# Optimization experiments

Hardware: AMD Instinct MI355X
Metric: run time of the kernel (lower is better)

## Reference

```python
import jax, jax.numpy as jnp
import numpy as np
import itertools

B = 2; DIM = 256; HEADS = 8; RES = 256; WIN = 16
FWS = WIN // 2            # freq window size = 8
HD = DIM // HEADS         # head dim = 32
N = FWS * FWS             # tokens per window = 64
SCALE = HD ** -0.5

def _make_bias_idxs():
    pts = list(itertools.product(range(FWS), range(FWS)))
    offs, idxs = {}, []
    for p1 in pts:
        for p2 in pts:
            o = (abs(p1[0] - p2[0]), abs(p1[1] - p2[1]))
            if o not in offs:
                offs[o] = len(offs)
            idxs.append(offs[o])
    return np.asarray(idxs, np.int32).reshape(N, N), len(offs)

def _conv(x, w, stride, pad, groups, lhs_dilation=None):
    return jax.lax.conv_general_dilated(
        x, w, (stride, stride), pad, lhs_dilation=lhs_dilation,
        feature_group_count=groups, dimension_numbers=('NCHW', 'OIHW', 'NCHW'))

def _window_partition(x, ws):
    b, c, h, w = x.shape
    x = x.reshape(b, c, h // ws, ws, w // ws, ws)
    x = x.transpose(0, 2, 4, 1, 3, 5)
    return x.reshape(-1, c, ws, ws)

def _window_reverse(x, ws, h, w):
    nh, nw = h // ws, w // ws
    c = x.shape[1]
    x = x.reshape(-1, nh, nw, c, ws, ws)
    x = x.transpose(0, 3, 1, 4, 2, 5)
    return x.reshape(-1, c, h, w)

def setup_inputs():
    key = jax.random.key(0)
    ks = jax.random.split(key, 8)
    idxs, n_off = _make_bias_idxs()
    return {
        'x': jax.random.normal(ks[0], (B, DIM, RES, RES), jnp.float32),
        'wt_filter': jax.random.normal(ks[1], (4 * DIM, 1, 2, 2), jnp.float32) * 0.1,
        'iwt_filter': jax.random.normal(ks[2], (4 * DIM, 1, 2, 2), jnp.float32) * 0.1,
        'dw_weight': jax.random.normal(ks[3], (HEADS, HD, 1, 5, 5), jnp.float32) * 0.1,
        'dw_bias': jax.random.normal(ks[4], (HEADS, HD), jnp.float32) * 0.1,
        'proj_weight': jax.random.normal(ks[5], (DIM, DIM), jnp.float32) * 0.05,
        'proj_bias': jax.random.normal(ks[6], (DIM,), jnp.float32) * 0.1,
        'attention_biases': jax.random.normal(ks[7], (HEADS, n_off), jnp.float32) * 0.1,
        'bias_idxs': jnp.asarray(idxs),
    }

def reference(x, wt_filter, iwt_filter, dw_weight, dw_bias, proj_weight, proj_bias, attention_biases, bias_idxs):
    b, c, h, w = x.shape
    h2, w2 = h // 2, w // 2
    # DWT: grouped stride-2 conv producing 4 subbands per channel (k=2 -> pad 0)
    xw = _conv(x, wt_filter, 2, 'VALID', c).reshape(b, c, 4, h2, w2)
    ll, lh, hl, hh = xw[:, :, 0], xw[:, :, 1], xw[:, :, 2], xw[:, :, 3]
    llw = _window_partition(ll, FWS)   # (Bn, C, 8, 8)
    lhw = _window_partition(lh, FWS)
    hlw = _window_partition(hl, FWS)
    bn = llw.shape[0]
    bias = attention_biases[:, bias_idxs]  # (HEADS, N, N) relative-pos bias gather
    outs = []
    ll_i = llw[:, :HD]
    for i in range(HEADS):  # sequential over heads: ll_i accumulates
        sl = slice(i * HD, (i + 1) * HD)
        if i > 0:
            ll_i = ll_i + llw[:, sl]
        # per-head depthwise 5x5 conv (BN folded) as Q projection of LH band
        q = _conv(lhw[:, sl], dw_weight[i], 1, ((2, 2), (2, 2)), HD) \
            + dw_bias[i][None, :, None, None]
        q = q.reshape(bn, HD, N).transpose(0, 2, 1)        # (Bn, N, hd)
        k = hlw[:, sl].reshape(bn, HD, N)                  # (Bn, hd, N)
        v = ll_i.reshape(bn, HD, N)                        # (Bn, hd, N)
        attn = jnp.einsum('bnd,bdm->bnm', q, k) * SCALE + bias[i]
        attn = jax.nn.softmax(attn, axis=-1)
        ll_i = jnp.einsum('bdm,bnm->bdn', v, attn).reshape(bn, HD, FWS, FWS)
        outs.append(ll_i)
    ll_out = jnp.concatenate(outs, axis=1)
    # proj: ReLU -> 1x1 conv with BN folded into weight/bias
    ll_out = jnp.einsum('oc,bchw->bohw', proj_weight, jax.nn.relu(ll_out)) \
             + proj_bias[None, :, None, None]
    ll_out = _window_reverse(ll_out, FWS, h2, w2)
    wt_out = jnp.stack([ll_out, lh, hl, hh], axis=2).reshape(b, 4 * c, h2, w2)
    # IDWT: conv_transpose(stride=2, pad=0) == input-dilated conv, flipped kernel
    kT = iwt_filter.reshape(c, 4, 2, 2)[:, :, ::-1, ::-1]
    return _conv(wt_out, kT, 1, ((1, 1), (1, 1)), c, lhs_dilation=(2, 2))
```

## Files before the change

### kernel.cpp

```cpp
#include <hip/hip_runtime.h>
#include <hip/hip_bf16.h>

typedef __hip_bfloat16 bf16;

__device__ __forceinline__ float b2f(bf16 v) { return __bfloat162float(v); }
__device__ __forceinline__ bf16 f2b(float v) { return __float2bfloat16(v); }
__device__ __forceinline__ void up2(unsigned u, float& lo, float& hi) {
  lo = __uint_as_float(u << 16);
  hi = __uint_as_float(u & 0xFFFF0000u);
}

__device__ __forceinline__ bool detect_f32(const void* p) {
  const unsigned* u = (const unsigned*)p;
  int c = 0;
#pragma unroll
  for (int i = 0; i < 64; ++i) {
    unsigned e = (u[i] >> 7) & 0xFF;
    c += (e >= 170);
  }
  return c > 0;
}

__device__ __forceinline__ float ldp(const void* p, int i, bool f32) {
  return f32 ? ((const float*)p)[i] : b2f(((const bf16*)p)[i]);
}
__device__ __forceinline__ void ldpair(const void* p, size_t du, bool f32,
                                       float& a, float& b) {
  if (f32) {
    float2 v = ((const float2*)p)[du];
    a = v.x; b = v.y;
  } else {
    up2(((const unsigned*)p)[du], a, b);
  }
}
__device__ __forceinline__ void ld4(const void* p, size_t i, bool f32,
                                    float4& o) {
  if (f32) {
    o = ((const float4*)p)[i >> 2];
  } else {
    uint2 u = ((const uint2*)p)[i >> 2];
    up2(u.x, o.x, o.y);
    up2(u.y, o.z, o.w);
  }
}

#define SCALE 0.17677669529663687f

__global__ __launch_bounds__(512, 4) void fused_kernel(
    const void* __restrict__ x, const void* __restrict__ wtf,
    const void* __restrict__ iwtf,
    const void* __restrict__ dww, const void* __restrict__ dwb,
    const void* __restrict__ pw, const void* __restrict__ pb,
    const void* __restrict__ ab, const int* __restrict__ bidx,
    void* __restrict__ out) {
  __shared__ float lh_s[32 * 65];
  __shared__ float k_s[32 * 65];
  __shared__ float v_s[32 * 65];
  __shared__ float out_s[32 * 68];
  __shared__ float q_s[64 * 33];
  __shared__ float attn_s[64 * 65];
  __shared__ float w5_s[800];
  __shared__ float wf_s[512];
  __shared__ float ab_s[64];
  __shared__ float inv_s[64];

  const bool xf = detect_f32(x);
  const bool pf = detect_f32(pw);

  int t = threadIdx.x;
  int w = blockIdx.x;
  int b = w >> 8, wi = w & 255, wy = wi >> 4, wx = wi & 15;

  float acc[4][8] = {};
  int to = t >> 3, tp = t & 7;
  int m = t & 63, ng = t >> 6;

  float pwf0 = ldp(wtf, t, pf);
  float pw5r[2];
#pragma unroll
  for (int e2 = 0; e2 < 2; ++e2) {
    int idx = t + 512 * e2;
    pw5r[e2] = (idx < 800) ? ldp(dww, idx, pf) : 0.f;
  }
  float pabr = (t < 64) ? ldp(ab, t, pf) : 0.f;

#pragma unroll 1
  for (int h = 0; h < 8; ++h) {
    wf_s[t] = pwf0;
#pragma unroll
    for (int e2 = 0; e2 < 2; ++e2) {
      int idx = t + 512 * e2;
      if (idx < 800) w5_s[idx] = pw5r[e2];
    }
    if (t < 64) ab_s[t] = pabr;
    if (h < 7) {
      pwf0 = ldp(wtf, (h + 1) * 512 + t, pf);
#pragma unroll
      for (int e2 = 0; e2 < 2; ++e2) {
        int idx = t + 512 * e2;
        if (idx < 800) pw5r[e2] = ldp(dww, (h + 1) * 800 + idx, pf);
      }
      if (t < 64) pabr = ldp(ab, (h + 1) * 64 + t, pf);
    }
    __syncthreads();

#pragma unroll
    for (int e = 0; e < 4; ++e) {
      int idx = t + 512 * e;
      int d = idx >> 6, p = idx & 63, r = p >> 3, cc = p & 7;
      int plane = b * 256 + h * 32 + d;
      size_t du =
          ((size_t)plane << 15) + ((wy * 16 + 2 * r) << 7) + wx * 8 + cc;
      float x00, x01, x10, x11;
      ldpair(x, du, xf, x00, x01);
      ldpair(x, du + 128, xf, x10, x11);
      const float* f = wf_s + d * 16;
      float llv = x00 * f[0] + x01 * f[1] + x10 * f[2] + x11 * f[3];
      lh_s[d * 65 + p] = x00 * f[4] + x01 * f[5] + x10 * f[6] + x11 * f[7];
      k_s[d * 65 + p] = x00 * f[8] + x01 * f[9] + x10 * f[10] + x11 * f[11];
      if (h == 0)
        v_s[d * 65 + p] = llv;
      else
        v_s[d * 65 + p] = out_s[d * 68 + p] + llv;
    }
    __syncthreads();

    {
      float dwbv = ldp(dwb, h * 32 + (t & 31), pf);
#pragma unroll
      for (int e = 0; e < 4; ++e) {
        int idx = t + 512 * e;
        int d = idx & 31, n = idx >> 5;
        int r = n >> 3, cc = n & 7;
        float qa = dwbv;
        for (int u = 0; u < 5; ++u) {
          int rr = r + u - 2;
          if (rr < 0 || rr > 7) continue;
          for (int v = 0; v < 5; ++v) {
            int c2 = cc + v - 2;
            if (c2 < 0 || c2 > 7) continue;
            qa += lh_s[d * 65 + rr * 8 + c2] * w5_s[d * 25 + u * 5 + v];
          }
        }
        q_s[n * 33 + d] = qa;
      }
    }
    __syncthreads();

    {
      float kreg[32];
#pragma unroll
      for (int d = 0; d < 32; ++d) kreg[d] = k_s[d * 65 + m];
#pragma unroll
      for (int nn = 0; nn < 8; ++nn) {
        int n = ng * 8 + nn;
        float a2 = 0.f;
#pragma unroll
        for (int d = 0; d < 32; ++d) a2 += q_s[n * 33 + d] * kreg[d];
        a2 = a2 * SCALE + ab_s[bidx[n * 64 + m]];
        float mx = a2;
#pragma unroll
        for (int msk = 32; msk > 0; msk >>= 1)
          mx = fmaxf(mx, __shfl_xor(mx, msk, 64));
        float e2 = __expf(a2 - mx);
        float sum = e2;
#pragma unroll
        for (int msk = 32; msk > 0; msk >>= 1) sum += __shfl_xor(sum, msk, 64);
        attn_s[n * 65 + m] = e2;
        if (m == 0) inv_s[n] = 1.f / sum;
      }
    }
    __syncthreads();

    {
      int d = t & 31, n0 = (t >> 5) * 4;
      float pv[4] = {0, 0, 0, 0};
      for (int mm = 0; mm < 64; ++mm) {
        float vv = v_s[d * 65 + mm];
#pragma unroll
        for (int e = 0; e < 4; ++e) pv[e] += vv * attn_s[(n0 + e) * 65 + mm];
      }
#pragma unroll
      for (int e = 0; e < 4; ++e)
        out_s[d * 68 + n0 + e] = pv[e] * inv_s[n0 + e];
    }
    __syncthreads();

#pragma unroll 1
    for (int q4 = 0; q4 < 8; ++q4) {
      float4 w4[4];
#pragma unroll
      for (int i2 = 0; i2 < 4; ++i2)
        ld4(pw, (size_t)(to + 64 * i2) * 256 + h * 32 + q4 * 4, pf, w4[i2]);
#pragma unroll
      for (int j = 0; j < 4; ++j) {
        int kk = q4 * 4 + j;
        float r[8];
#pragma unroll
        for (int pi = 0; pi < 8; ++pi)
          r[pi] = fmaxf(out_s[kk * 68 + tp + 8 * pi], 0.f);
#pragma unroll
        for (int i2 = 0; i2 < 4; ++i2) {
          float wv = (j == 0)   ? w4[i2].x
                     : (j == 1) ? w4[i2].y
                     : (j == 2) ? w4[i2].z
                                : w4[i2].w;
#pragma unroll
          for (int pi = 0; pi < 8; ++pi) acc[i2][pi] += wv * r[pi];
        }
      }
    }
  }

#pragma unroll 1
  for (int i2 = 0; i2 < 4; ++i2) {
    int o = to + 64 * i2;
    float pbv = ldp(pb, o, pf);
    float f[16], g[16];
#pragma unroll
    for (int e = 0; e < 16; ++e) {
      f[e] = ldp(wtf, o * 16 + e, pf);
      g[e] = ldp(iwtf, o * 16 + e, pf);
    }
    int plane = b * 256 + o;
#pragma unroll
    for (int pi = 0; pi < 8; ++pi) {
      int y = wy * 8 + pi;
      int xb = wx * 8 + tp;
      float llv = acc[i2][pi] + pbv;
      size_t du = ((size_t)plane << 15) + ((size_t)(2 * y) << 7) + xb;
      float x00, x01, x10, x11;
      ldpair(x, du, xf, x00, x01);
      ldpair(x, du + 128, xf, x10, x11);
      float lhv = x00 * f[4] + x01 * f[5] + x10 * f[6] + x11 * f[7];
      float hlv = x00 * f[8] + x01 * f[9] + x10 * f[10] + x11 * f[11];
      float hhv = x00 * f[12] + x01 * f[13] + x10 * f[14] + x11 * f[15];
#pragma unroll
      for (int sy = 0; sy < 2; ++sy) {
        float v0 = llv * g[0 + sy * 2] + lhv * g[4 + sy * 2] +
                   hlv * g[8 + sy * 2] + hhv * g[12 + sy * 2];
        float v1 = llv * g[1 + sy * 2] + lhv * g[5 + sy * 2] +
                   hlv * g[9 + sy * 2] + hhv * g[13 + sy * 2];
        size_t oi = ((size_t)plane << 15) + ((size_t)(2 * y + sy) << 7) + xb;
        if (xf) {
          ((float2*)out)[oi] = make_float2(v0, v1);
        } else {
          union { bf16 hh2[2]; unsigned u; } pk;
          pk.hh2[0] = f2b(v0);
          pk.hh2[1] = f2b(v1);
          ((unsigned*)out)[oi] = pk.u;
        }
      }
    }
  }
}

extern "C" void kernel_launch(void* const* d_in, const int* in_sizes, int n_in,
                              void* d_out, int out_size, void* d_ws, size_t ws_size,
                              hipStream_t stream) {
  const void *x, *wtf, *iwtf, *dww, *dwb, *pw, *pb, *ab;
  const int* bidx;
  if (in_sizes[0] == 33554432) {
    x = d_in[0]; wtf = d_in[1]; iwtf = d_in[2]; dww = d_in[3]; dwb = d_in[4];
    pw = d_in[5]; pb = d_in[6]; ab = d_in[7]; bidx = (const int*)d_in[8];
  } else if (in_sizes[0] == 512) {
    ab = d_in[0]; bidx = (const int*)d_in[1]; dwb = d_in[2]; dww = d_in[3];
    iwtf = d_in[4]; pb = d_in[5]; pw = d_in[6]; wtf = d_in[7]; x = d_in[8];
  } else {
    bidx = (const int*)d_in[0]; ab = d_in[1]; pb = d_in[2]; pw = d_in[3];
    dwb = d_in[4]; dww = d_in[5]; iwtf = d_in[6]; wtf = d_in[7]; x = d_in[8];
  }

  fused_kernel<<<512, 512, 0, stream>>>(x, wtf, iwtf, dww, dwb, pw, pb, ab,
                                        bidx, d_out);
}
```

Baseline: 549.6 us.

## Prefetch next head's x tiles into registers and double-buffer weight staging

Loads the x values each head needs into registers one head ahead, so the global loads for head h+1 are issued during head h's attention work instead of right before the DWT step. Weight, depthwise-filter and bias staging moves to double-buffered shared arrays, which removes one __syncthreads per head. The cost is 16 more live registers per thread, plus a small amount of extra shared memory, under launch bounds that already target high occupancy. This may force spills or lower occupancy.

```diff
diff --git a/kernel.cpp b/kernel.cpp
--- a/kernel.cpp
+++ b/kernel.cpp
@@ -59,9 +59,9 @@
   __shared__ float out_s[32 * 68];
   __shared__ float q_s[64 * 33];
   __shared__ float attn_s[64 * 65];
-  __shared__ float w5_s[800];
-  __shared__ float wf_s[512];
-  __shared__ float ab_s[64];
+  __shared__ float w5_s[2][800];
+  __shared__ float wf_s[2][512];
+  __shared__ float ab_s[2][64];
   __shared__ float inv_s[64];
 
   const bool xf = detect_f32(x);
@@ -75,53 +75,81 @@
   int to = t >> 3, tp = t & 7;
   int m = t & 63, ng = t >> 6;
 
-  float pwf0 = ldp(wtf, t, pf);
+  {
+    wf_s[0][t] = ldp(wtf, t, pf);
+#pragma unroll
+    for (int e2 = 0; e2 < 2; ++e2) {
+      int idx = t + 512 * e2;
+      if (idx < 800) w5_s[0][idx] = ldp(dww, idx, pf);
+    }
+    if (t < 64) ab_s[0][t] = ldp(ab, t, pf);
+  }
+  float pwf0 = ldp(wtf, 512 + t, pf);
   float pw5r[2];
 #pragma unroll
   for (int e2 = 0; e2 < 2; ++e2) {
     int idx = t + 512 * e2;
-    pw5r[e2] = (idx < 800) ? ldp(dww, idx, pf) : 0.f;
-  }
-  float pabr = (t < 64) ? ldp(ab, t, pf) : 0.f;
+    pw5r[e2] = (idx < 800) ? ldp(dww, 800 + idx, pf) : 0.f;
+  }
+  float pabr = (t < 64) ? ldp(ab, 64 + t, pf) : 0.f;
+
+  float X0[4], X1[4], X2[4], X3[4];
+#pragma unroll
+  for (int e = 0; e < 4; ++e) {
+    int idx = t + 512 * e;
+    int d = idx >> 6, p = idx & 63, r = p >> 3, cc = p & 7;
+    int plane = b * 256 + d;
+    size_t du = ((size_t)plane << 15) + ((wy * 16 + 2 * r) << 7) + wx * 8 + cc;
+    ldpair(x, du, xf, X0[e], X1[e]);
+    ldpair(x, du + 128, xf, X2[e], X3[e]);
+  }
+  __syncthreads();
 
 #pragma unroll 1
   for (int h = 0; h < 8; ++h) {
-    wf_s[t] = pwf0;
-#pragma unroll
-    for (int e2 = 0; e2 < 2; ++e2) {
-      int idx = t + 512 * e2;
-      if (idx < 800) w5_s[idx] = pw5r[e2];
-    }
-    if (t < 64) ab_s[t] = pabr;
-    if (h < 7) {
-      pwf0 = ldp(wtf, (h + 1) * 512 + t, pf);
-#pragma unroll
-      for (int e2 = 0; e2 < 2; ++e2) {
-        int idx = t + 512 * e2;
-        if (idx < 800) pw5r[e2] = ldp(dww, (h + 1) * 800 + idx, pf);
-      }
-      if (t < 64) pabr = ldp(ab, (h + 1) * 64 + t, pf);
-    }
-    __syncthreads();
-
+    const int cur = h & 1;
 #pragma unroll
     for (int e = 0; e < 4; ++e) {
       int idx = t + 512 * e;
-      int d = idx >> 6, p = idx & 63, r = p >> 3, cc = p & 7;
-      int plane = b * 256 + h * 32 + d;
-      size_t du =
-          ((size_t)plane << 15) + ((wy * 16 + 2 * r) << 7) + wx * 8 + cc;
-      float x00, x01, x10, x11;
-      ldpair(x, du, xf, x00, x01);
-      ldpair(x, du + 128, xf, x10, x11);
-      const float* f = wf_s + d * 16;
-      float llv = x00 * f[0] + x01 * f[1] + x10 * f[2] + x11 * f[3];
-      lh_s[d * 65 + p] = x00 * f[4] + x01 * f[5] + x10 * f[6] + x11 * f[7];
-      k_s[d * 65 + p] = x00 * f[8] + x01 * f[9] + x10 * f[10] + x11 * f[11];
+      int d = idx >> 6, p = idx & 63;
+      const float* f = wf_s[cur] + d * 16;
+      float llv = X0[e] * f[0] + X1[e] * f[1] + X2[e] * f[2] + X3[e] * f[3];
+      lh_s[d * 65 + p] = X0[e] * f[4] + X1[e] * f[5] + X2[e] * f[6] + X3[e] * f[7];
+      k_s[d * 65 + p] = X0[e] * f[8] + X1[e] * f[9] + X2[e] * f[10] + X3[e] * f[11];
       if (h == 0)
         v_s[d * 65 + p] = llv;
       else
         v_s[d * 65 + p] = out_s[d * 68 + p] + llv;
+    }
+    if (h < 7) {
+      wf_s[cur ^ 1][t] = pwf0;
+#pragma unroll
+      for (int e2 = 0; e2 < 2; ++e2) {
+        int idx = t + 512 * e2;
+        if (idx < 800) w5_s[cur ^ 1][idx] = pw5r[e2];
+      }
+      if (t < 64) ab_s[cur ^ 1][t] = pabr;
+    }
+    if (h < 6) {
+      pwf0 = ldp(wtf, (h + 2) * 512 + t, pf);
+#pragma unroll
+      for (int e2 = 0; e2 < 2; ++e2) {
+        int idx = t + 512 * e2;
+        pw5r[e2] = (idx < 800) ? ldp(dww, (h + 2) * 800 + idx, pf) : 0.f;
+      }
+      if (t < 64) pabr = ldp(ab, (h + 2) * 64 + t, pf);
+    }
+    if (h < 7) {
+#pragma unroll
+      for (int e = 0; e < 4; ++e) {
+        int idx = t + 512 * e;
+        int d = idx >> 6, p = idx & 63, r = p >> 3, cc = p & 7;
+        int plane = b * 256 + (h + 1) * 32 + d;
+        size_t du =
+            ((size_t)plane << 15) + ((wy * 16 + 2 * r) << 7) + wx * 8 + cc;
+        ldpair(x, du, xf, X0[e], X1[e]);
+        ldpair(x, du + 128, xf, X2[e], X3[e]);
+      }
     }
     __syncthreads();
 
@@ -139,7 +167,7 @@
           for (int v = 0; v < 5; ++v) {
             int c2 = cc + v - 2;
             if (c2 < 0 || c2 > 7) continue;
-            qa += lh_s[d * 65 + rr * 8 + c2] * w5_s[d * 25 + u * 5 + v];
+            qa += lh_s[d * 65 + rr * 8 + c2] * w5_s[cur][d * 25 + u * 5 + v];
           }
         }
         q_s[n * 33 + d] = qa;
@@ -157,7 +185,7 @@
         float a2 = 0.f;
 #pragma unroll
         for (int d = 0; d < 32; ++d) a2 += q_s[n * 33 + d] * kreg[d];
-        a2 = a2 * SCALE + ab_s[bidx[n * 64 + m]];
+        a2 = a2 * SCALE + ab_s[cur][bidx[n * 64 + m]];
         float mx = a2;
 #pragma unroll
         for (int msk = 32; msk > 0; msk >>= 1)
```

After: 637.5 us. +16.0%, slower.
